# Performance work log

Measured on AMD Instinct MI355X. Metric: run time of the kernel, lower is better.

The kernel has to match this reference:

```python
import jax, jax.numpy as jnp
import numpy as np

N_BINS = 18
TEMP = 0.01  # n_phases > 1e7 so effective_temperature = 0.01 (same as init default)
EPS = 1e-10  # fp16=False
PI = np.pi


def setup_inputs() -> dict:
    key = jax.random.key(0)
    k1, k2 = jax.random.split(key)
    B, C, P, A, S, T = 4, 8, 20, 30, 4, 2048
    phase = jax.random.uniform(k1, (B, C, P, S, T), jnp.float32, -PI, PI)
    amplitude = jax.random.uniform(k2, (B, C, A, S, T), jnp.float32, 0.0, 1.0)
    return {"phase": phase, "amplitude": amplitude}


def reference(phase, amplitude):
    # phase:     (B, C, Fp, S, T)
    # amplitude: (B, C, Fa, S, T)
    edges = jnp.linspace(-PI, PI, N_BINS + 1).astype(phase.dtype)
    centers = (edges[1:] + edges[:-1]) * 0.5  # (N,)

    # Soft phase binning: circular distance to each bin center, softmax over bins.
    diff = phase[..., None] - centers  # (B, C, Fp, S, T, N)
    diff = jnp.fmod(diff + PI, 2.0 * PI) - PI  # torch.fmod = truncated mod = jnp.fmod
    weights = jax.nn.softmax(-jnp.abs(diff) / TEMP, axis=-1)  # (B, C, Fp, S, T, N)

    # Amplitude-weighted histogram: contract over time.
    # dist: (B, C, Fp, Fa, S, N)
    dist = jnp.einsum('bcpstn,bcast->bcpasn', weights, amplitude)

    # Normalize to a distribution over bins, clamp, Shannon entropy.
    p = dist / (dist.sum(axis=-1, keepdims=True) + EPS)
    p = jnp.maximum(p, EPS)
    neg_entropy = (p * jnp.log(p)).sum(axis=-1)  # (B, C, Fp, Fa, S)

    mi = 1.0 + neg_entropy / jnp.log(jnp.asarray(N_BINS, dtype=p.dtype))
    # -> (B, C, S, Fp, Fa) to match torch output layout
    return jnp.transpose(mi, (0, 1, 4, 2, 3))
```

## Files before the change

kernel.cpp:

```cpp
#include <hip/hip_runtime.h>
#include <math.h>
#include <stdint.h>

#define BB 4
#define CC 8
#define PP 20
#define AA 30
#define SS 4
#define TT 2048
#define NB 18

#define TC 128
#define NCH (TT / TC)
#define PG 2
#define NPG (PP / PG)
#define WSTR 132
#define WROWS 19
#define NTH 256

#define BAR() do { asm volatile("s_waitcnt lgkmcnt(0)" ::: "memory"); \
                   __builtin_amdgcn_s_barrier(); } while (0)

typedef _Float16 half4_t __attribute__((ext_vector_type(4)));
typedef _Float16 half8_t __attribute__((ext_vector_type(8)));
typedef float f32x16 __attribute__((ext_vector_type(16)));

__device__ __forceinline__ void weight_top2(float x, int& n0, int& n1,
                                            float& w0, float& w1)
{
    const float PI_F  = 3.14159265358979323846f;
    const float INV_H = 2.8647913f;
    float u = (x + PI_F) * INV_H;
    n0 = (int)floorf(u);
    n0 = n0 < 0 ? 0 : (n0 > NB - 1 ? NB - 1 : n0);
    float f  = u - (float)n0 - 0.5f;
    float af = fabsf(f);
    n1 = n0 + (f >= 0.0f ? 1 : -1);
    float e;
    if (n1 < 0) {
        e = 0.0f; n1 = NB;
    } else {
        if (n1 == NB) n1 = 0;
        e = __expf(fmaf(af, 69.81317008f, -34.90658504f));
    }
    w0 = __builtin_amdgcn_rcpf(1.0f + e);
    w1 = 1.0f - w0;
}

__global__ __launch_bounds__(NTH, 5)
void mi_fused_kernel(const float* __restrict__ phase,
                     const float* __restrict__ amp,
                     float* __restrict__ out)
{
    __shared__ __align__(16) _Float16 Wl[PG][WROWS * WSTR];
    __shared__ __align__(16) _Float16 ampT[2][AA * WSTR];

    const int tid = threadIdx.x;
    const int bid = blockIdx.x;
    const int x   = bid & 7;
    const int kk  = bid >> 3;
    const int pg  = kk % NPG;
    const int g   = x + 8 * (kk / NPG);
    const int s   = g & (SS - 1);
    const int bc  = g >> 2;

    const int w    = tid >> 6;
    const int wv   = w & 1;
    const int kh   = w >> 1;
    const int lane = tid & 63;
    const int mrow = lane & 31;
    const int mlh  = lane >> 5;
    const int arow = mrow < WROWS ? mrow : (WROWS - 1);
    const int brow = mrow < AA    ? mrow : (AA - 1);
    const int col  = kh * 64 + lane;

    const int p = pg * PG + wv;
    const float* am  = amp   + (size_t)bc * (AA * SS * TT) + (size_t)s * TT;
    const float* phw = phase + ((size_t)(bc * PP + p) * SS + s) * TT;
    float*       op  = out   + ((size_t)(bc * SS + s) * PP + p) * AA;

    for (int i = tid; i < 2 * 627; i += NTH)
        ((uint2*)Wl)[i] = make_uint2(0u, 0u);
    #pragma unroll
    for (int j = 0; j < 4; ++j) {
        int q = tid + j * NTH;
        int a = q >> 5, tq = q & 31;
        if (a < AA) {
            const float4 v = *(const float4*)&am[(size_t)a * (SS * TT) + tq * 4];
            half4_t h = { (_Float16)v.x, (_Float16)v.y, (_Float16)v.z, (_Float16)v.w };
            *(half4_t*)&ampT[0][a * WSTR + tq * 4] = h;
        }
    }
    float phv = phw[col];
    BAR();

    f32x16 acc0 = {}, acc1 = {};
    int pn0 = 0, pn1 = 0;

    for (int c = 0; c < NCH; ++c) {
        const int cb = c & 1, tb = cb ^ 1;

        float nphv = 0.0f;
        float4 stg[4];
        if (c + 1 < NCH) {
            nphv = phw[(c + 1) * TC + col];
            #pragma unroll
            for (int j = 0; j < 4; ++j) {
                int q = tid + j * NTH;
                int a = q >> 5, tq = q & 31;
                int ac = a < AA ? a : (AA - 1);
                stg[j] = *(const float4*)&am[(size_t)ac * (SS * TT) + (c + 1) * TC + tq * 4];
            }
        }

        if (c > 0) {
            Wl[wv][pn0 * WSTR + col] = (_Float16)0.0f;
            Wl[wv][pn1 * WSTR + col] = (_Float16)0.0f;
        }
        {
            int n0, n1; float w0, w1;
            weight_top2(phv, n0, n1, w0, w1);
            Wl[wv][n0 * WSTR + col] = (_Float16)w0;
            Wl[wv][n1 * WSTR + col] = (_Float16)w1;
            pn0 = n0; pn1 = n1;
        }

        __builtin_amdgcn_s_setprio(1);
        #pragma unroll
        for (int ks = 0; ks < 4; ++ks) {
            int t0 = kh * 64 + ks * 16 + mlh * 8;
            const _Float16* Ab = &Wl[wv][arow * WSTR + t0];
            const _Float16* Bb = &ampT[cb][brow * WSTR + t0];
            half4_t a0 = *(const half4_t*)Ab;
            half4_t a1 = *(const half4_t*)(Ab + 4);
            half4_t b0 = *(const half4_t*)Bb;
            half4_t b1 = *(const half4_t*)(Bb + 4);
            half8_t av = __builtin_shufflevector(a0, a1, 0, 1, 2, 3, 4, 5, 6, 7);
            half8_t bv = __builtin_shufflevector(b0, b1, 0, 1, 2, 3, 4, 5, 6, 7);
            if (ks & 1) acc1 = __builtin_amdgcn_mfma_f32_32x32x16_f16(av, bv, acc1, 0, 0, 0);
            else        acc0 = __builtin_amdgcn_mfma_f32_32x32x16_f16(av, bv, acc0, 0, 0, 0);
        }
        __builtin_amdgcn_s_setprio(0);

        if (c + 1 < NCH) {
            #pragma unroll
            for (int j = 0; j < 4; ++j) {
                int q = tid + j * NTH;
                int a = q >> 5, tq = q & 31;
                if (a < AA) {
                    half4_t h = { (_Float16)stg[j].x, (_Float16)stg[j].y,
                                  (_Float16)stg[j].z, (_Float16)stg[j].w };
                    *(half4_t*)&ampT[tb][a * WSTR + tq * 4] = h;
                }
            }
        }
        phv = nphv;
        BAR();
    }

    f32x16 acc = acc0 + acc1;
    float* dmp = (float*)((char*)&Wl[wv][0] + kh * 2376);
    #pragma unroll
    for (int r = 0; r < 16; ++r) {
        int row = (r & 3) + 8 * (r >> 2) + 4 * mlh;
        if (row < NB) dmp[row * 33 + mrow] = acc[r];
    }
    BAR();

    if (kh == 0 && lane < AA) {
        const float* d0 = (const float*)&Wl[wv][0];
        const float* d1 = (const float*)((char*)&Wl[wv][0] + 2376);
        float v[NB], tot = 0.0f;
        #pragma unroll
        for (int n = 0; n < NB; ++n) {
            v[n] = d0[n * 33 + lane] + d1[n * 33 + lane];
            tot += v[n];
        }
        float inv = 1.0f / (tot + 1e-10f);
        float ne = 0.0f;
        #pragma unroll
        for (int n = 0; n < NB; ++n) {
            float pv = fmaxf(v[n] * inv, 1e-10f);
            ne += pv * logf(pv);
        }
        op[lane] = 1.0f + ne * 0.345975362f;
    }
}

extern "C" void kernel_launch(void* const* d_in, const int* in_sizes, int n_in,
                              void* d_out, int out_size, void* d_ws, size_t ws_size,
                              hipStream_t stream)
{
    const float* phase = (const float*)d_in[0];
    const float* amp   = (const float*)d_in[1];
    float* out = (float*)d_out;
    hipLaunchKernelGGL(mi_fused_kernel, dim3(BB * CC * SS * NPG), dim3(NTH),
                       0, stream, phase, amp, out);
}
```

Measured before the change: 29.00 us.

## Share amplitude B-fragment across both phase tiles per wave, split time among four waves

```diff
diff --git a/kernel.cpp b/kernel.cpp
--- a/kernel.cpp
+++ b/kernel.cpp
@@ -52,8 +52,10 @@
                      const float* __restrict__ amp,
                      float* __restrict__ out)
 {
-    __shared__ __align__(16) _Float16 Wl[PG][WROWS * WSTR];
-    __shared__ __align__(16) _Float16 ampT[2][AA * WSTR];
+    __shared__ __align__(16) _Float16 lds[2 * WROWS * WSTR + 2 * AA * WSTR];
+    _Float16* const Wl0 = lds;
+    _Float16* const Wl1 = lds + WROWS * WSTR;
+    _Float16* const amp0 = lds + 2 * WROWS * WSTR;
 
     const int tid = threadIdx.x;
     const int bid = blockIdx.x;
@@ -64,23 +66,20 @@
     const int s   = g & (SS - 1);
     const int bc  = g >> 2;
 
-    const int w    = tid >> 6;
-    const int wv   = w & 1;
-    const int kh   = w >> 1;
+    const int kh   = tid >> 6;
     const int lane = tid & 63;
     const int mrow = lane & 31;
     const int mlh  = lane >> 5;
     const int arow = mrow < WROWS ? mrow : (WROWS - 1);
     const int brow = mrow < AA    ? mrow : (AA - 1);
-    const int col  = kh * 64 + lane;
-
-    const int p = pg * PG + wv;
-    const float* am  = amp   + (size_t)bc * (AA * SS * TT) + (size_t)s * TT;
-    const float* phw = phase + ((size_t)(bc * PP + p) * SS + s) * TT;
-    float*       op  = out   + ((size_t)(bc * SS + s) * PP + p) * AA;
-
-    for (int i = tid; i < 2 * 627; i += NTH)
-        ((uint2*)Wl)[i] = make_uint2(0u, 0u);
+    const int col  = kh * 32 + mrow;
+    _Float16* const ptile = mlh ? Wl1 : Wl0;
+
+    const float* am  = amp + (size_t)bc * (AA * SS * TT) + (size_t)s * TT;
+    const float* phl = phase + ((size_t)(bc * PP + pg * PG + mlh) * SS + s) * TT + col;
+
+    for (int i = tid; i < 627; i += NTH)
+        ((uint4*)lds)[i] = make_uint4(0u, 0u, 0u, 0u);
     #pragma unroll
     for (int j = 0; j < 4; ++j) {
         int q = tid + j * NTH;
@@ -88,10 +87,10 @@
         if (a < AA) {
             const float4 v = *(const float4*)&am[(size_t)a * (SS * TT) + tq * 4];
             half4_t h = { (_Float16)v.x, (_Float16)v.y, (_Float16)v.z, (_Float16)v.w };
-            *(half4_t*)&ampT[0][a * WSTR + tq * 4] = h;
-        }
-    }
-    float phv = phw[col];
+            *(half4_t*)&amp0[a * WSTR + tq * 4] = h;
+        }
+    }
+    float phv = phl[0];
     BAR();
 
     f32x16 acc0 = {}, acc1 = {};
@@ -99,11 +98,13 @@
 
     for (int c = 0; c < NCH; ++c) {
         const int cb = c & 1, tb = cb ^ 1;
+        const _Float16* aB = amp0 + cb * (AA * WSTR);
+        _Float16* aW = amp0 + tb * (AA * WSTR);
 
         float nphv = 0.0f;
         float4 stg[4];
         if (c + 1 < NCH) {
-            nphv = phw[(c + 1) * TC + col];
+            nphv = phl[(c + 1) * TC];
             #pragma unroll
             for (int j = 0; j < 4; ++j) {
                 int q = tid + j * NTH;
@@ -114,31 +115,35 @@
         }
 
         if (c > 0) {
-            Wl[wv][pn0 * WSTR + col] = (_Float16)0.0f;
-            Wl[wv][pn1 * WSTR + col] = (_Float16)0.0f;
+            ptile[pn0 * WSTR + col] = (_Float16)0.0f;
+            ptile[pn1 * WSTR + col] = (_Float16)0.0f;
         }
         {
             int n0, n1; float w0, w1;
             weight_top2(phv, n0, n1, w0, w1);
-            Wl[wv][n0 * WSTR + col] = (_Float16)w0;
-            Wl[wv][n1 * WSTR + col] = (_Float16)w1;
+            ptile[n0 * WSTR + col] = (_Float16)w0;
+            ptile[n1 * WSTR + col] = (_Float16)w1;
             pn0 = n0; pn1 = n1;
         }
 
         __builtin_amdgcn_s_setprio(1);
         #pragma unroll
-        for (int ks = 0; ks < 4; ++ks) {
-            int t0 = kh * 64 + ks * 16 + mlh * 8;
-            const _Float16* Ab = &Wl[wv][arow * WSTR + t0];
-            const _Float16* Bb = &ampT[cb][brow * WSTR + t0];
-            half4_t a0 = *(const half4_t*)Ab;
-            half4_t a1 = *(const half4_t*)(Ab + 4);
+        for (int ks = 0; ks < 2; ++ks) {
+            int t0 = kh * 32 + ks * 16 + mlh * 8;
+            const _Float16* Bb  = aB  + brow * WSTR + t0;
+            const _Float16* A0b = Wl0 + arow * WSTR + t0;
+            const _Float16* A1b = Wl1 + arow * WSTR + t0;
             half4_t b0 = *(const half4_t*)Bb;
             half4_t b1 = *(const half4_t*)(Bb + 4);
-            half8_t av = __builtin_shufflevector(a0, a1, 0, 1, 2, 3, 4, 5, 6, 7);
-            half8_t bv = __builtin_shufflevector(b0, b1, 0, 1, 2, 3, 4, 5, 6, 7);
-            if (ks & 1) acc1 = __builtin_amdgcn_mfma_f32_32x32x16_f16(av, bv, acc1, 0, 0, 0);
-            else        acc0 = __builtin_amdgcn_mfma_f32_32x32x16_f16(av, bv, acc0, 0, 0, 0);
+            half4_t p0a = *(const half4_t*)A0b;
+            half4_t p0b = *(const half4_t*)(A0b + 4);
+            half4_t p1a = *(const half4_t*)A1b;
+            half4_t p1b = *(const half4_t*)(A1b + 4);
+            half8_t bv  = __builtin_shufflevector(b0, b1, 0, 1, 2, 3, 4, 5, 6, 7);
+            half8_t a0v = __builtin_shufflevector(p0a, p0b, 0, 1, 2, 3, 4, 5, 6, 7);
+            half8_t a1v = __builtin_shufflevector(p1a, p1b, 0, 1, 2, 3, 4, 5, 6, 7);
+            acc0 = __builtin_amdgcn_mfma_f32_32x32x16_f16(a0v, bv, acc0, 0, 0, 0);
+            acc1 = __builtin_amdgcn_mfma_f32_32x32x16_f16(a1v, bv, acc1, 0, 0, 0);
         }
         __builtin_amdgcn_s_setprio(0);
 
@@ -150,7 +155,7 @@
                 if (a < AA) {
                     half4_t h = { (_Float16)stg[j].x, (_Float16)stg[j].y,
                                   (_Float16)stg[j].z, (_Float16)stg[j].w };
-                    *(half4_t*)&ampT[tb][a * WSTR + tq * 4] = h;
+                    *(half4_t*)&aW[a * WSTR + tq * 4] = h;
                 }
             }
         }
@@ -158,22 +163,25 @@
         BAR();
     }
 
-    f32x16 acc = acc0 + acc1;
-    float* dmp = (float*)((char*)&Wl[wv][0] + kh * 2376);
+    float* const df = (float*)lds;
     #pragma unroll
     for (int r = 0; r < 16; ++r) {
         int row = (r & 3) + 8 * (r >> 2) + 4 * mlh;
-        if (row < NB) dmp[row * 33 + mrow] = acc[r];
+        if (row < NB) {
+            df[(kh * 2 + 0) * 576 + row * 32 + mrow] = acc0[r];
+            df[(kh * 2 + 1) * 576 + row * 32 + mrow] = acc1[r];
+        }
     }
     BAR();
 
-    if (kh == 0 && lane < AA) {
-        const float* d0 = (const float*)&Wl[wv][0];
-        const float* d1 = (const float*)((char*)&Wl[wv][0] + 2376);
+    if (kh < PG && lane < AA) {
         float v[NB], tot = 0.0f;
         #pragma unroll
         for (int n = 0; n < NB; ++n) {
-            v[n] = d0[n * 33 + lane] + d1[n * 33 + lane];
+            v[n] = df[(0 * 2 + kh) * 576 + n * 32 + lane]
+                 + df[(1 * 2 + kh) * 576 + n * 32 + lane]
+                 + df[(2 * 2 + kh) * 576 + n * 32 + lane]
+                 + df[(3 * 2 + kh) * 576 + n * 32 + lane];
             tot += v[n];
         }
         float inv = 1.0f / (tot + 1e-10f);
@@ -183,7 +191,8 @@
             float pv = fmaxf(v[n] * inv, 1e-10f);
             ne += pv * logf(pv);
         }
-        op[lane] = 1.0f + ne * 0.345975362f;
+        out[((size_t)(bc * SS + s) * PP + pg * PG + kh) * AA + lane] =
+            1.0f + ne * 0.345975362f;
     }
 }
 
```

Result: faster. 28.21 us, median of 2 (-2.7%).
